# Optimization experiments

Measured on AMD Instinct MI355X. Metric: run time of the kernel, lower is better.

The kernel has to match this reference:

```python
import jax, jax.numpy as jnp
import numpy as np

START_IDX = 1  # PAD_IDX = 0, END_IDX = 2 (unused in teacher-forcing path)
B, N, F = 16, 49, 1024
H, E, V = 1024, 1024, 15000
S, W = 5, 12


def setup_inputs() -> dict:
    key = jax.random.key(0)
    ks = jax.random.split(key, 16)
    def w(k, shape, s=0.02):
        return jax.random.normal(k, shape, dtype=jnp.float32) * s
    emb = w(ks[0], (V, E)).at[0].set(0.0)  # padding_idx = 0
    return dict(
        features=jax.random.normal(ks[1], (B, N, F), dtype=jnp.float32),
        reports=jax.random.randint(ks[2], (B, S, W), 0, V),
        attn_w1=w(ks[3], (F + H, H)), attn_b1=jnp.zeros((H,), jnp.float32),
        attn_w2=w(ks[4], (H, 1)), attn_b2=jnp.zeros((1,), jnp.float32),
        s_wih=w(ks[5], (4 * H, F)), s_whh=w(ks[6], (4 * H, H)),
        s_bih=jnp.zeros((4 * H,), jnp.float32), s_bhh=jnp.zeros((4 * H,), jnp.float32),
        stop_w=w(ks[7], (H, 1)), stop_b=jnp.zeros((1,), jnp.float32),
        emb=emb,
        w_wih=w(ks[8], (4 * H, E)), w_whh=w(ks[9], (4 * H, H)),
        w_bih=jnp.zeros((4 * H,), jnp.float32), w_bhh=jnp.zeros((4 * H,), jnp.float32),
        fc_w=w(ks[10], (H, V)), fc_b=jnp.zeros((V,), jnp.float32),
    )


def _lstm_cell(x, h, c, wih, whh, bih, bhh):
    # PyTorch LSTMCell: gates ordered i, f, g, o
    gates = x @ wih.T + h @ whh.T + (bih + bhh)
    i, f, g, o = jnp.split(gates, 4, axis=-1)
    c = jax.nn.sigmoid(f) * c + jax.nn.sigmoid(i) * jnp.tanh(g)
    h = jax.nn.sigmoid(o) * jnp.tanh(c)
    return h, c


def _attention(features, h, w1, b1, w2, b2):
    # features [B,N,F], h [B,H] -> additive 2-layer attention over N locations
    b, n, _ = features.shape
    hcat = jnp.broadcast_to(h[:, None, :], (b, n, h.shape[-1]))
    x = jnp.concatenate([features, hcat], axis=-1)           # [B,N,F+H]
    e = (jnp.tanh(x @ w1 + b1) @ w2 + b2)[..., 0]            # [B,N]
    scores = jax.nn.softmax(e, axis=-1)
    att = jnp.einsum('bn,bnf->bf', scores, features)          # [B,F]
    return att, scores


def _forward(features, reports, attn_w1, attn_b1, attn_w2, attn_b2,
             s_wih, s_whh, s_bih, s_bhh, stop_w, stop_b, emb,
             w_wih, w_whh, w_bih, w_bhh, fc_w, fc_b):
    bsz = features.shape[0]
    h0 = jnp.zeros((bsz, s_whh.shape[-1]), features.dtype)
    att0, _ = _attention(features, h0, attn_w1, attn_b1, attn_w2, attn_b2)
    start_emb = jnp.broadcast_to(emb[START_IDX][None, :], (bsz, emb.shape[-1]))

    def sentence_step(carry, reports_i):   # reports_i: [W, B] teacher-forcing tokens
        h, c, att = carry
        h, c = _lstm_cell(att, h, c, s_wih, s_whh, s_bih, s_bhh)
        czero = jnp.zeros_like(h)

        def word_step(wc, idx):
            hw, cw, inp = wc
            hw, cw = _lstm_cell(inp, hw, cw, w_wih, w_whh, w_bih, w_bhh)
            pred = hw @ fc_w + fc_b                           # [B,V]
            return (hw, cw, emb[idx]), pred

        # word LSTM initialized with h=topic, c=0; first input = <start> embedding
        _, preds = jax.lax.scan(word_step, (h, czero, start_emb), reports_i)  # [W,B,V]
        stop = jax.nn.sigmoid(h @ stop_w + stop_b)[:, 0]      # [B]
        att, scores = _attention(features, h, attn_w1, attn_b1, attn_w2, attn_b2)
        return (h, c, att), (preds, stop, scores)

    reports_sw = jnp.transpose(reports, (1, 2, 0))            # [S,W,B]
    _, (seq, stops, scores) = jax.lax.scan(sentence_step, (h0, h0, att0), reports_sw)
    seq_out = jnp.transpose(seq, (2, 0, 1, 3))                # [B,S,W,V]
    stops_out = jnp.transpose(stops, (1, 0))                  # [B,S]
    scores_out = jnp.transpose(scores, (1, 0, 2))             # [B,S,N]
    return seq_out, stops_out, scores_out


def reference(features, reports, attn_w1, attn_b1, attn_w2, attn_b2,
              s_wih, s_whh, s_bih, s_bhh, stop_w, stop_b, emb,
              w_wih, w_whh, w_bih, w_bhh, fc_w, fc_b):
    return _forward(features, reports, attn_w1, attn_b1, attn_w2, attn_b2,
                    s_wih, s_whh, s_bih, s_bhh, stop_w, stop_b, emb,
                    w_wih, w_whh, w_bih, w_bhh, fc_w, fc_b)
```

## Files before the change

kernel.cpp:

```cpp
#include <hip/hip_runtime.h>
#include <hip/hip_bf16.h>

#define B_  16
#define S_  5
#define W_  12
#define NL_ 49
#define H_  1024
#define V_  15000
#define SEQ_N   14400000
#define STOP_N  80
#define OUT_STOP (SEQ_N)
#define OUT_SCORE (SEQ_N + STOP_N)

typedef __attribute__((ext_vector_type(8))) short     short8;
typedef __attribute__((ext_vector_type(4))) float     f32x4;
typedef __attribute__((ext_vector_type(4))) unsigned int u32x4;
typedef __attribute__((ext_vector_type(4))) unsigned short us4;

#define OFF_FCWT   0ull
#define OFF_WWHHP  30720000ull
#define OFF_WWIHP  39108608ull
#define OFF_WSCATP 47497216ull
#define OFF_W1AT   64274432ull
#define OFF_W1BT   66371584ull
#define OFF_FBF    68468736ull
#define OFF_XIN    70074368ull
#define OFF_PF     72040448ull
#define OFF_XW     75251712ull
#define OFF_HBALL  90980352ull
#define OFF_HWBF0  92946432ull
#define OFF_HWBF1  93110272ull
#define OFF_ACAT1  93274112ull
#define OFF_H      93339648ull
#define OFF_EVAL   93405184ull
#define OFF_ACAT0  93408384ull
#define OFF_C      93473920ull
#define OFF_CW     93539456ull
#define OFF_HPROJ  93867136ull
#define WS_TOTAL   93932672ull
#define ZERO_BASE  OFF_ACAT0
#define ZERO_BYTES (524288ull)

__device__ __forceinline__ unsigned short f2bf(float x){
  unsigned u = __float_as_uint(x);
  u += 0x7fffu + ((u >> 16) & 1u);
  return (unsigned short)(u >> 16);
}
__device__ __forceinline__ float sigm(float x){ return 1.f/(1.f+expf(-x)); }

typedef __attribute__((address_space(3))) unsigned int  as3_u32;
typedef __attribute__((address_space(1))) const unsigned int as1_u32;

__device__ __forceinline__ void gl16(const void* g, void* l){
  __builtin_amdgcn_global_load_lds((as1_u32*)g, (as3_u32*)l, 16, 0, 0);
}

template<int ROWS,int CH,int NW>
__device__ __forceinline__ void stage_swz(const unsigned short* __restrict__ gbase, int grs,
                                          unsigned short* lds, int wid, int lane,
                                          int r0, int rmax){
  constexpr int RPI = 64/CH;
  constexpr int NISS = ROWS/RPI;
  const int r_in = lane / CH;
  const int cbp  = lane % CH;
  #pragma unroll
  for (int it = wid; it < NISS; it += NW){
    int rl = it*RPI + r_in;
    int gr = r0 + rl; gr = gr < rmax ? gr : rmax-1;
    int cb = cbp ^ (rl & 7);
    gl16(gbase + (size_t)gr*grs + cb*8, lds + it*RPI*CH*8);
  }
}

__global__ void k_cvt(const float* __restrict__ src, unsigned short* __restrict__ dst, int n){
  int idx = (blockIdx.x*256 + threadIdx.x)*4;
  if (idx >= n) return;
  f32x4 v = *(const f32x4*)(src + idx);
  us4 o; o[0]=f2bf(v[0]); o[1]=f2bf(v[1]); o[2]=f2bf(v[2]); o[3]=f2bf(v[3]);
  *(us4*)(dst + idx) = o;
}

__global__ void k_cvt_gate(const float* __restrict__ src, unsigned short* __restrict__ dst,
                           int dld, int doff){
  int idx = (blockIdx.x*256 + threadIdx.x)*4;
  int n = idx >> 10, cc = idx & 1023;
  int gate = (n >> 4) & 3, j = ((n >> 6) << 4) | (n & 15);
  f32x4 v = *(const f32x4*)(src + ((size_t)(gate*1024 + j) << 10) + cc);
  us4 o; o[0]=f2bf(v[0]); o[1]=f2bf(v[1]); o[2]=f2bf(v[2]); o[3]=f2bf(v[3]);
  *(us4*)(dst + (size_t)n*dld + doff + cc) = o;
}

__global__ void k_transp(const float* __restrict__ src, int sld, int r0, int R, int Cc,
                         unsigned short* __restrict__ dst, int dld){
  __shared__ float t[32][33];
  int rb = blockIdx.x*32, cb = blockIdx.y*32;
  int tx = threadIdx.x & 31, ty = threadIdx.x >> 5;
  for (int i = ty; i < 32; i += 8){
    int r = rb + i, c = cb + tx;
    t[i][tx] = (r < R && c < Cc) ? src[(size_t)(r0 + r)*sld + c] : 0.f;
  }
  __syncthreads();
  for (int i = ty; i < 32; i += 8){
    int c = cb + i, r = rb + tx;
    if (c < Cc && r < R) dst[(size_t)c*dld + r] = f2bf(t[tx][i]);
  }
}

__global__ void k_gather(const float* __restrict__ emb, const int* __restrict__ reports,
                         unsigned short* __restrict__ Xin){
  int m = blockIdx.x;
  int w = m / 80, r = m % 80, s = r >> 4, b = r & 15;
  int tok = (w == 0) ? 1 : reports[b*60 + s*12 + (w-1)];
  const float* src = emb + ((size_t)tok << 10);
  int k = threadIdx.x * 4;
  f32x4 v = *(const f32x4*)(src + k);
  us4 o; o[0]=f2bf(v[0]); o[1]=f2bf(v[1]); o[2]=f2bf(v[2]); o[3]=f2bf(v[3]);
  *(us4*)(Xin + (size_t)m*1024 + k) = o;
}

template<int BM,int BN,int BK,int WM,int WN,int EPI>
__global__ void k_gemm(const unsigned short* __restrict__ A, int lda,
                       const unsigned short* __restrict__ Bt, int ldb,
                       float* __restrict__ C, int ldc,
                       const float* __restrict__ bias,
                       int M, int N, int K)
{
  constexpr int NWV = WM*WN;
  constexpr int CH = BK/8;
  __shared__ __align__(16) unsigned short As[BM*BK];
  __shared__ __align__(16) unsigned short Bs[BN*BK];
  const int n0 = blockIdx.x * BN, m0 = blockIdx.y * BM;
  if (n0 >= N) return;
  const int tid  = threadIdx.x;
  const int lane = tid & 63;
  const int wave = tid >> 6;
  constexpr int WROWS = BM/WM, WCOLS = BN/WN;
  constexpr int FM = WROWS/16, FN = WCOLS/16;
  const int wm = wave / WN, wn = wave % WN;
  const int g = lane >> 4, fr = lane & 15;
  const int sx = fr & 7;

  f32x4 acc[FM][FN];
  #pragma unroll
  for (int a=0;a<FM;a++)
    #pragma unroll
    for (int b=0;b<FN;b++) acc[a][b] = (f32x4){0.f,0.f,0.f,0.f};

  for (int k0 = 0; k0 < K; k0 += BK) {
    if (k0) __syncthreads();
    stage_swz<BM,CH,NWV>(A + k0, lda, As, wave, lane, m0, M);
    stage_swz<BN,CH,NWV>(Bt + k0, ldb, Bs, wave, lane, n0, N);
    __syncthreads();
    #pragma unroll
    for (int kk = 0; kk < BK; kk += 32) {
      const int so = ((kk/8 + g) ^ sx) * 8;
      short8 af[FM], bt[FN];
      #pragma unroll
      for (int fm=0; fm<FM; fm++)
        af[fm] = *(const short8*)(As + (wm*WROWS + fm*16 + fr)*BK + so);
      #pragma unroll
      for (int fn=0; fn<FN; fn++)
        bt[fn] = *(const short8*)(Bs + (wn*WCOLS + fn*16 + fr)*BK + so);
      #pragma unroll
      for (int fm=0; fm<FM; fm++)
        #pragma unroll
        for (int fn=0; fn<FN; fn++)
          acc[fm][fn] = __builtin_amdgcn_mfma_f32_16x16x32_bf16(af[fm], bt[fn], acc[fm][fn], 0, 0, 0);
    }
  }

  #pragma unroll
  for (int fm=0; fm<FM; fm++)
    #pragma unroll
    for (int fn=0; fn<FN; fn++)
      #pragma unroll
      for (int j=0; j<4; j++){
        int m = m0 + wm*WROWS + fm*16 + g*4 + j;
        int n = n0 + wn*WCOLS + fn*16 + fr;
        if (m < M && n < N) {
          float v = acc[fm][fn][j];
          if (EPI == 1 || EPI == 2) v += bias[n];
          if (EPI == 2) {
            int b = m & 15, s = (m >> 4) % 5, w = m / 80;
            __builtin_nontemporal_store(v, &C[(size_t)((b*5 + s)*12 + w)*V_ + n]);
          } else if (EPI == 3) {
            __builtin_nontemporal_store(v, &C[(size_t)m*ldc + n]);
          } else {
            C[(size_t)m*ldc + n] = v;
          }
        }
      }
}

template<int BM,int BN,int BK,int WN,int SENT>
__global__ void k_gemm_cell(const unsigned short* __restrict__ A, int lda,
                            const unsigned short* __restrict__ Bt, int ldb,
                            const float* __restrict__ Xg, int ldx,
                            const float* __restrict__ bih, const float* __restrict__ bhh,
                            float* __restrict__ cst,
                            unsigned short* __restrict__ h1, int ldh1,
                            unsigned short* __restrict__ h2,
                            float* __restrict__ hf,
                            int M, int K)
{
  constexpr int CH = BK/8;
  __shared__ __align__(16) unsigned short As[BM*BK];
  __shared__ __align__(16) unsigned short Bs[BN*BK];
  const int tid  = threadIdx.x;
  const int lane = tid & 63;
  const int wn   = tid >> 6;
  const int n0 = blockIdx.x * BN, m0 = blockIdx.y * BM;
  const int g = lane >> 4, fr = lane & 15;
  const int sx = fr & 7;

  f32x4 acc[4];
  #pragma unroll
  for (int b=0;b<4;b++) acc[b] = (f32x4){0.f,0.f,0.f,0.f};

  for (int k0 = 0; k0 < K; k0 += BK) {
    if (k0) __syncthreads();
    stage_swz<BM,CH,WN>(A + k0, lda, As, wn, lane, m0, M);
    stage_swz<BN,CH,WN>(Bt + k0, ldb, Bs, wn, lane, n0, 4096);
    __syncthreads();
    #pragma unroll
    for (int kk = 0; kk < BK; kk += 32) {
      const int so = ((kk/8 + g) ^ sx) * 8;
      short8 af = *(const short8*)(As + fr*BK + so);
      #pragma unroll
      for (int fn=0; fn<4; fn++){
        short8 bt = *(const short8*)(Bs + (wn*64 + fn*16 + fr)*BK + so);
        acc[fn] = __builtin_amdgcn_mfma_f32_16x16x32_bf16(af, bt, acc[fn], 0, 0, 0);
      }
    }
  }

  const int nb = n0 + wn*64 + fr;
  const int j  = ((n0 + wn*64) >> 2) + fr;
  const float b0 = bih[j]        + bhh[j];
  const float b1 = bih[1024 + j] + bhh[1024 + j];
  const float b2 = bih[2048 + j] + bhh[2048 + j];
  const float b3 = bih[3072 + j] + bhh[3072 + j];
  #pragma unroll
  for (int jj=0; jj<4; jj++){
    int m = m0 + g*4 + jj;
    if (m < M){
      float gi = acc[0][jj] + b0;
      float gf = acc[1][jj] + b1;
      float gg = acc[2][jj] + b2;
      float go = acc[3][jj] + b3;
      if (!SENT){
        const float* xg = Xg + (size_t)m*ldx + nb;
        gi += xg[0]; gf += xg[16]; gg += xg[32]; go += xg[48];
      }
      float cn = sigm(gf)*cst[m*1024 + j] + sigm(gi)*tanhf(gg);
      float hn = sigm(go)*tanhf(cn);
      cst[m*1024 + j] = cn;
      unsigned short hb = f2bf(hn);
      h1[(size_t)m*ldh1 + j] = hb;
      h2[(size_t)m*1024 + j] = hb;
      if (SENT) hf[m*1024 + j] = hn;
    }
  }
}

__global__ void k_attn_e(const float* __restrict__ PF, const float* __restrict__ hproj,
                         const float* __restrict__ w2, float* __restrict__ evals)
{
  const int bn = blockIdx.x;
  const int b  = bn / NL_;
  const int tid = threadIdx.x;
  __shared__ float red[4];
  const float* pf = PF + ((size_t)bn << 10);
  const float* hp = hproj + (b << 10);
  int k = tid * 4;
  f32x4 a = *(const f32x4*)(pf + k);
  f32x4 hh = *(const f32x4*)(hp + k);
  f32x4 w = *(const f32x4*)(w2 + k);
  float p = tanhf(a[0]+hh[0])*w[0] + tanhf(a[1]+hh[1])*w[1]
          + tanhf(a[2]+hh[2])*w[2] + tanhf(a[3]+hh[3])*w[3];
  #pragma unroll
  for (int o = 32; o; o >>= 1) p += __shfl_down(p, o, 64);
  if ((tid & 63) == 0) red[tid >> 6] = p;
  __syncthreads();
  if (tid == 0) evals[bn] = red[0] + red[1] + red[2] + red[3];
}

template<int INIT>
__global__ void k_attn_fin(const float* __restrict__ evals, const float* __restrict__ features,
                           const float* __restrict__ h, const float* __restrict__ stop_w,
                           const float* __restrict__ stop_b,
                           unsigned short* __restrict__ Acat, float* __restrict__ outp, int s)
{
  const int b = blockIdx.x, tid = threadIdx.x;
  __shared__ float scs[64];
  __shared__ float red[4];
  if (tid < 64){
    float e = (tid < NL_) ? evals[b*NL_ + tid] : -1e30f;
    float mx = e;
    #pragma unroll
    for (int o = 32; o; o >>= 1) mx = fmaxf(mx, __shfl_xor(mx, o, 64));
    float ex = (tid < NL_) ? expf(e - mx) : 0.f;
    float dn = ex;
    #pragma unroll
    for (int o = 32; o; o >>= 1) dn += __shfl_xor(dn, o, 64);
    float sc = ex / dn;
    if (tid < NL_){
      scs[tid] = sc;
      if (!INIT) outp[OUT_SCORE + (b*5 + s)*NL_ + tid] = sc;
    }
  }
  __syncthreads();
  {
    int f0 = tid * 4;
    f32x4 a = (f32x4){0.f,0.f,0.f,0.f};
    const float* fb = features + (((size_t)b*NL_) << 10) + f0;
    #pragma unroll 7
    for (int n = 0; n < NL_; n++){
      f32x4 v = *(const f32x4*)(fb + ((size_t)n << 10));
      float sc = scs[n];
      a[0] += sc*v[0]; a[1] += sc*v[1]; a[2] += sc*v[2]; a[3] += sc*v[3];
    }
    us4 o4; o4[0]=f2bf(a[0]); o4[1]=f2bf(a[1]); o4[2]=f2bf(a[2]); o4[3]=f2bf(a[3]);
    *(us4*)(Acat + b*2048 + f0) = o4;
  }
  if (!INIT){
    int k = tid * 4;
    f32x4 hv = *(const f32x4*)(h + (b << 10) + k);
    f32x4 sw = *(const f32x4*)(stop_w + k);
    float p = hv[0]*sw[0] + hv[1]*sw[1] + hv[2]*sw[2] + hv[3]*sw[3];
    #pragma unroll
    for (int o = 32; o; o >>= 1) p += __shfl_down(p, o, 64);
    if ((tid & 63) == 0) red[tid >> 6] = p;
    __syncthreads();
    if (tid == 0) outp[OUT_STOP + b*5 + s] = sigm(red[0]+red[1]+red[2]+red[3] + stop_b[0]);
  }
}

extern "C" void kernel_launch(void* const* d_in, const int* in_sizes, int n_in,
                              void* d_out, int out_size, void* d_ws, size_t ws_size,
                              hipStream_t stream)
{
  const float* features = (const float*)d_in[0];
  const int*   reports  = (const int*)d_in[1];
  const float* attn_w1  = (const float*)d_in[2];
  const float* attn_b1  = (const float*)d_in[3];
  const float* attn_w2  = (const float*)d_in[4];
  const float* s_wih    = (const float*)d_in[6];
  const float* s_whh    = (const float*)d_in[7];
  const float* s_bih    = (const float*)d_in[8];
  const float* s_bhh    = (const float*)d_in[9];
  const float* stop_w   = (const float*)d_in[10];
  const float* stop_b   = (const float*)d_in[11];
  const float* emb      = (const float*)d_in[12];
  const float* w_wih    = (const float*)d_in[13];
  const float* w_whh    = (const float*)d_in[14];
  const float* w_bih    = (const float*)d_in[15];
  const float* w_bhh    = (const float*)d_in[16];
  const float* fc_w     = (const float*)d_in[17];
  const float* fc_b     = (const float*)d_in[18];
  float* out = (float*)d_out;
  char*  ws  = (char*)d_ws;
  if (ws_size < WS_TOTAL) return;

  unsigned short* FCWT   = (unsigned short*)(ws + OFF_FCWT);
  unsigned short* WWHHP  = (unsigned short*)(ws + OFF_WWHHP);
  unsigned short* WWIHP  = (unsigned short*)(ws + OFF_WWIHP);
  unsigned short* WSCATP = (unsigned short*)(ws + OFF_WSCATP);
  unsigned short* W1AT   = (unsigned short*)(ws + OFF_W1AT);
  unsigned short* W1BT   = (unsigned short*)(ws + OFF_W1BT);
  unsigned short* FBF    = (unsigned short*)(ws + OFF_FBF);
  unsigned short* XIN    = (unsigned short*)(ws + OFF_XIN);
  float*          PF     = (float*)(ws + OFF_PF);
  float*          XW     = (float*)(ws + OFF_XW);
  unsigned short* HBALL  = (unsigned short*)(ws + OFF_HBALL);
  unsigned short* HW0    = (unsigned short*)(ws + OFF_HWBF0);
  unsigned short* HW1    = (unsigned short*)(ws + OFF_HWBF1);
  unsigned short* ACAT0  = (unsigned short*)(ws + OFF_ACAT0);
  unsigned short* ACAT1  = (unsigned short*)(ws + OFF_ACAT1);
  float*          Hst    = (float*)(ws + OFF_H);
  float*          Cst    = (float*)(ws + OFF_C);
  float*          CW     = (float*)(ws + OFF_CW);
  float*          HPROJ  = (float*)(ws + OFF_HPROJ);
  float*          EVAL   = (float*)(ws + OFF_EVAL);

  hipMemsetAsync(ws + ZERO_BASE, 0, ZERO_BYTES, stream);

  k_cvt<<<784, 256, 0, stream>>>(features, FBF, 802816);
  k_cvt_gate<<<4096, 256, 0, stream>>>(w_whh, WWHHP, 1024, 0);
  k_cvt_gate<<<4096, 256, 0, stream>>>(w_wih, WWIHP, 1024, 0);
  k_cvt_gate<<<4096, 256, 0, stream>>>(s_wih, WSCATP, 2048, 0);
  k_cvt_gate<<<4096, 256, 0, stream>>>(s_whh, WSCATP, 2048, 1024);
  k_transp<<<dim3(32,32),  256, 0, stream>>>(attn_w1, 1024, 0,    1024, 1024,  W1AT, 1024);
  k_transp<<<dim3(32,32),  256, 0, stream>>>(attn_w1, 1024, 1024, 1024, 1024,  W1BT, 1024);
  k_transp<<<dim3(32,469), 256, 0, stream>>>(fc_w,   15000, 0,    1024, 15000, FCWT, 1024);
  k_gather<<<960, 256, 0, stream>>>(emb, reports, XIN);

  k_gemm<64,64,128,2,2,1><<<dim3(16,13), 256, 0, stream>>>(FBF,1024, W1AT,1024, PF,1024, attn_b1, 784,1024,1024);
  k_gemm<64,128,128,2,2,3><<<dim3(32,15), 256, 0, stream>>>(XIN,1024, WWIHP,1024, XW,4096, nullptr, 960,4096,1024);

  k_attn_e<<<784, 256, 0, stream>>>(PF, HPROJ, attn_w2, EVAL);
  k_attn_fin<1><<<16, 256, 0, stream>>>(EVAL, features, Hst, stop_w, stop_b, ACAT0, out, 0);

  unsigned short* ACS[2] = {ACAT0, ACAT1};
  for (int s = 0; s < S_; s++){
    unsigned short* cur = ACS[s & 1];
    unsigned short* nxt = ACS[(s + 1) & 1];
    k_gemm_cell<16,128,128,2,1><<<dim3(32,1), 128, 0, stream>>>(
        cur, 2048, WSCATP, 2048, nullptr, 0, s_bih, s_bhh, Cst,
        nxt + 1024, 2048, HW0 + s*16*1024, Hst, 16, 2048);
    k_gemm<16,64,256,1,4,0><<<dim3(16,1), 256, 0, stream>>>(
        nxt + 1024, 2048, W1BT, 1024, HPROJ, 1024, nullptr, 16, 1024, 1024);
    k_attn_e<<<784, 256, 0, stream>>>(PF, HPROJ, attn_w2, EVAL);
    k_attn_fin<0><<<16, 256, 0, stream>>>(EVAL, features, Hst, stop_w, stop_b, nxt, out, s);
  }

  unsigned short* HW[2] = {HW0, HW1};
  for (int w = 0; w < W_; w++){
    k_gemm_cell<16,128,128,2,0><<<dim3(32,5), 128, 0, stream>>>(
        HW[w & 1], 1024, WWHHP, 1024, XW + (size_t)w*80*4096, 4096, w_bih, w_bhh, CW,
        HW[(w + 1) & 1], 1024, HBALL + (size_t)w*80*1024, nullptr, 80, 1024);
  }

  k_gemm<128,128,64,2,2,2><<<dim3(120,8), 256, 0, stream>>>(HBALL,1024, FCWT,1024, out,V_, fc_b, 960,15000,1024);
}
```

Measured before the change: 559.1 us.

## Fuse prep kernels and run word LSTM as persistent kernel with grid barrier

Merges the feature, gate-weight and embedding conversion kernels into one launch and the two attn_w1 transposes into one. Replaces the 12 per-step word LSTM launches with one persistent kernel of 160 blocks that syncs through a global atomic barrier, whose counters are zeroed by the existing memset. Also changes the final FC GEMM tile shape and grid, and removes the n0 >= N early exit from k_gemm. The barrier assumes all 160 blocks are resident at once and adds spin-wait cost in exchange for removing launch gaps.

Measured after the change: 658.9 us. 17.9% more time.

```diff
diff --git a/kernel.cpp b/kernel.cpp
--- a/kernel.cpp
+++ b/kernel.cpp
@@ -37,9 +37,10 @@
 #define OFF_C      93473920ull
 #define OFF_CW     93539456ull
 #define OFF_HPROJ  93867136ull
-#define WS_TOTAL   93932672ull
+#define OFF_BAR    93932672ull
+#define WS_TOTAL   93932928ull
 #define ZERO_BASE  OFF_ACAT0
-#define ZERO_BYTES (524288ull)
+#define ZERO_BYTES (524544ull)
 
 __device__ __forceinline__ unsigned short f2bf(float x){
   unsigned u = __float_as_uint(x);
@@ -72,22 +73,74 @@
   }
 }
 
-__global__ void k_cvt(const float* __restrict__ src, unsigned short* __restrict__ dst, int n){
-  int idx = (blockIdx.x*256 + threadIdx.x)*4;
-  if (idx >= n) return;
-  f32x4 v = *(const f32x4*)(src + idx);
-  us4 o; o[0]=f2bf(v[0]); o[1]=f2bf(v[1]); o[2]=f2bf(v[2]); o[3]=f2bf(v[3]);
-  *(us4*)(dst + idx) = o;
-}
-
-__global__ void k_cvt_gate(const float* __restrict__ src, unsigned short* __restrict__ dst,
-                           int dld, int doff){
-  int idx = (blockIdx.x*256 + threadIdx.x)*4;
+__device__ __forceinline__ void gbar(unsigned* c, unsigned tgt){
+  __syncthreads();
+  if (threadIdx.x == 0){
+    __threadfence();
+    atomicAdd(c, 1u);
+    while (atomicAdd(c, 0u) < tgt) __builtin_amdgcn_s_sleep(8);
+    __threadfence();
+  }
+  __syncthreads();
+}
+
+__device__ __forceinline__ void cvt_gate_blk(const float* __restrict__ src,
+                                             unsigned short* __restrict__ dst,
+                                             int blk, int dld, int doff){
+  int idx = (blk*256 + threadIdx.x)*4;
   int n = idx >> 10, cc = idx & 1023;
   int gate = (n >> 4) & 3, j = ((n >> 6) << 4) | (n & 15);
   f32x4 v = *(const f32x4*)(src + ((size_t)(gate*1024 + j) << 10) + cc);
   us4 o; o[0]=f2bf(v[0]); o[1]=f2bf(v[1]); o[2]=f2bf(v[2]); o[3]=f2bf(v[3]);
   *(us4*)(dst + (size_t)n*dld + doff + cc) = o;
+}
+
+__global__ void k_prep(const float* __restrict__ features,
+                       const float* __restrict__ w_whh, const float* __restrict__ w_wih,
+                       const float* __restrict__ s_wih, const float* __restrict__ s_whh,
+                       const float* __restrict__ emb, const int* __restrict__ reports,
+                       unsigned short* __restrict__ FBF, unsigned short* __restrict__ WWHHP,
+                       unsigned short* __restrict__ WWIHP, unsigned short* __restrict__ WSCATP,
+                       unsigned short* __restrict__ XIN)
+{
+  int bx = blockIdx.x;
+  if (bx < 784){
+    int idx = (bx*256 + threadIdx.x)*4;
+    f32x4 v = *(const f32x4*)(features + idx);
+    us4 o; o[0]=f2bf(v[0]); o[1]=f2bf(v[1]); o[2]=f2bf(v[2]); o[3]=f2bf(v[3]);
+    *(us4*)(FBF + idx) = o;
+  } else if (bx < 784 + 4096){
+    cvt_gate_blk(w_whh, WWHHP, bx - 784, 1024, 0);
+  } else if (bx < 784 + 8192){
+    cvt_gate_blk(w_wih, WWIHP, bx - (784 + 4096), 1024, 0);
+  } else if (bx < 784 + 12288){
+    cvt_gate_blk(s_wih, WSCATP, bx - (784 + 8192), 2048, 0);
+  } else if (bx < 784 + 16384){
+    cvt_gate_blk(s_whh, WSCATP, bx - (784 + 12288), 2048, 1024);
+  } else {
+    int m = bx - (784 + 16384);
+    int w = m / 80, r = m % 80, s = r >> 4, b = r & 15;
+    int tok = (w == 0) ? 1 : reports[b*60 + s*12 + (w-1)];
+    const float* src = emb + ((size_t)tok << 10);
+    int k = threadIdx.x * 4;
+    f32x4 v = *(const f32x4*)(src + k);
+    us4 o; o[0]=f2bf(v[0]); o[1]=f2bf(v[1]); o[2]=f2bf(v[2]); o[3]=f2bf(v[3]);
+    *(us4*)(XIN + (size_t)m*1024 + k) = o;
+  }
+}
+
+__global__ void k_transp_w1(const float* __restrict__ src,
+                            unsigned short* __restrict__ W1AT, unsigned short* __restrict__ W1BT){
+  __shared__ float t[32][33];
+  unsigned short* dst = blockIdx.z ? W1BT : W1AT;
+  int r0 = blockIdx.z * 1024;
+  int rb = blockIdx.x*32, cb = blockIdx.y*32;
+  int tx = threadIdx.x & 31, ty = threadIdx.x >> 5;
+  for (int i = ty; i < 32; i += 8)
+    t[i][tx] = src[(size_t)(r0 + rb + i)*1024 + cb + tx];
+  __syncthreads();
+  for (int i = ty; i < 32; i += 8)
+    dst[(size_t)(cb + i)*1024 + rb + tx] = f2bf(t[tx][i]);
 }
 
 __global__ void k_transp(const float* __restrict__ src, int sld, int r0, int R, int Cc,
@@ -106,18 +159,6 @@
   }
 }
 
-__global__ void k_gather(const float* __restrict__ emb, const int* __restrict__ reports,
-                         unsigned short* __restrict__ Xin){
-  int m = blockIdx.x;
-  int w = m / 80, r = m % 80, s = r >> 4, b = r & 15;
-  int tok = (w == 0) ? 1 : reports[b*60 + s*12 + (w-1)];
-  const float* src = emb + ((size_t)tok << 10);
-  int k = threadIdx.x * 4;
-  f32x4 v = *(const f32x4*)(src + k);
-  us4 o; o[0]=f2bf(v[0]); o[1]=f2bf(v[1]); o[2]=f2bf(v[2]); o[3]=f2bf(v[3]);
-  *(us4*)(Xin + (size_t)m*1024 + k) = o;
-}
-
 template<int BM,int BN,int BK,int WM,int WN,int EPI>
 __global__ void k_gemm(const unsigned short* __restrict__ A, int lda,
                        const unsigned short* __restrict__ Bt, int ldb,
@@ -130,7 +171,6 @@
   __shared__ __align__(16) unsigned short As[BM*BK];
   __shared__ __align__(16) unsigned short Bs[BN*BK];
   const int n0 = blockIdx.x * BN, m0 = blockIdx.y * BM;
-  if (n0 >= N) return;
   const int tid  = threadIdx.x;
   const int lane = tid & 63;
   const int wave = tid >> 6;
@@ -192,16 +232,15 @@
       }
 }
 
-template<int BM,int BN,int BK,int WN,int SENT>
-__global__ void k_gemm_cell(const unsigned short* __restrict__ A, int lda,
-                            const unsigned short* __restrict__ Bt, int ldb,
-                            const float* __restrict__ Xg, int ldx,
-                            const float* __restrict__ bih, const float* __restrict__ bhh,
-                            float* __restrict__ cst,
-                            unsigned short* __restrict__ h1, int ldh1,
-                            unsigned short* __restrict__ h2,
-                            float* __restrict__ hf,
-                            int M, int K)
+template<int BM,int BN,int BK,int WN>
+__global__ void k_gemm_cell_s(const unsigned short* __restrict__ A, int lda,
+                              const unsigned short* __restrict__ Bt, int ldb,
+                              const float* __restrict__ bih, const float* __restrict__ bhh,
+                              float* __restrict__ cst,
+                              unsigned short* __restrict__ h1, int ldh1,
+                              unsigned short* __restrict__ h2,
+                              float* __restrict__ hf,
+                              int M, int K)
 {
   constexpr int CH = BK/8;
   __shared__ __align__(16) unsigned short As[BM*BK];
@@ -234,7 +273,6 @@
     }
   }
 
-  const int nb = n0 + wn*64 + fr;
   const int j  = ((n0 + wn*64) >> 2) + fr;
   const float b0 = bih[j]        + bhh[j];
   const float b1 = bih[1024 + j] + bhh[1024 + j];
@@ -248,18 +286,85 @@
       float gf = acc[1][jj] + b1;
       float gg = acc[2][jj] + b2;
       float go = acc[3][jj] + b3;
-      if (!SENT){
-        const float* xg = Xg + (size_t)m*ldx + nb;
-        gi += xg[0]; gf += xg[16]; gg += xg[32]; go += xg[48];
-      }
       float cn = sigm(gf)*cst[m*1024 + j] + sigm(gi)*tanhf(gg);
       float hn = sigm(go)*tanhf(cn);
       cst[m*1024 + j] = cn;
       unsigned short hb = f2bf(hn);
       h1[(size_t)m*ldh1 + j] = hb;
       h2[(size_t)m*1024 + j] = hb;
-      if (SENT) hf[m*1024 + j] = hn;
-    }
+      hf[m*1024 + j] = hn;
+    }
+  }
+}
+
+__global__ void __launch_bounds__(128) k_word_chain(
+    const unsigned short* __restrict__ Bt,
+    const float* __restrict__ XW,
+    const float* __restrict__ bih, const float* __restrict__ bhh,
+    float* __restrict__ cw,
+    unsigned short* __restrict__ HW0,
+    unsigned short* __restrict__ HW1,
+    unsigned short* __restrict__ Hball,
+    unsigned* __restrict__ bar)
+{
+  constexpr int BK = 128, CH = BK/8;
+  __shared__ __align__(16) unsigned short As[16*BK];
+  __shared__ __align__(16) unsigned short Bs[128*BK];
+  const int tid = threadIdx.x, lane = tid & 63, wn = tid >> 6;
+  const int n0 = blockIdx.x * 128, m0 = blockIdx.y * 16;
+  const int g = lane >> 4, fr = lane & 15, sx = fr & 7;
+  const unsigned tgt = 160;
+
+  const int nb = n0 + wn*64 + fr;
+  const int j  = ((n0 + wn*64) >> 2) + fr;
+  const float b0 = bih[j]        + bhh[j];
+  const float b1 = bih[1024 + j] + bhh[1024 + j];
+  const float b2 = bih[2048 + j] + bhh[2048 + j];
+  const float b3 = bih[3072 + j] + bhh[3072 + j];
+
+  unsigned short* HW[2] = {HW0, HW1};
+
+  for (int w = 0; w < W_; w++){
+    const unsigned short* A = HW[w & 1];
+    f32x4 acc[4];
+    #pragma unroll
+    for (int b=0;b<4;b++) acc[b] = (f32x4){0.f,0.f,0.f,0.f};
+
+    for (int k0 = 0; k0 < 1024; k0 += BK) {
+      if (k0) __syncthreads();
+      stage_swz<16,CH,2>(A + k0, 1024, As, wn, lane, m0, 80);
+      stage_swz<128,CH,2>(Bt + k0, 1024, Bs, wn, lane, n0, 4096);
+      __syncthreads();
+      #pragma unroll
+      for (int kk = 0; kk < BK; kk += 32) {
+        const int so = ((kk/8 + g) ^ sx) * 8;
+        short8 af = *(const short8*)(As + fr*BK + so);
+        #pragma unroll
+        for (int fn=0; fn<4; fn++){
+          short8 bt = *(const short8*)(Bs + (wn*64 + fn*16 + fr)*BK + so);
+          acc[fn] = __builtin_amdgcn_mfma_f32_16x16x32_bf16(af, bt, acc[fn], 0, 0, 0);
+        }
+      }
+    }
+
+    unsigned short* hnext = HW[(w + 1) & 1];
+    unsigned short* hb_out = Hball + (size_t)w*80*1024;
+    #pragma unroll
+    for (int jj=0; jj<4; jj++){
+      int m = m0 + g*4 + jj;
+      const float* xg = XW + (size_t)(w*80 + m)*4096 + nb;
+      float gi = acc[0][jj] + b0 + xg[0];
+      float gf = acc[1][jj] + b1 + xg[16];
+      float gg = acc[2][jj] + b2 + xg[32];
+      float go = acc[3][jj] + b3 + xg[48];
+      float cn = sigm(gf)*cw[m*1024 + j] + sigm(gi)*tanhf(gg);
+      float hn = sigm(go)*tanhf(cn);
+      cw[m*1024 + j] = cn;
+      unsigned short hb = f2bf(hn);
+      hnext[(size_t)m*1024 + j] = hb;
+      hb_out[(size_t)m*1024 + j] = hb;
+    }
+    if (w < W_ - 1) gbar(bar + w, tgt);
   }
 }
 
@@ -382,18 +487,14 @@
   float*          CW     = (float*)(ws + OFF_CW);
   float*          HPROJ  = (float*)(ws + OFF_HPROJ);
   float*          EVAL   = (float*)(ws + OFF_EVAL);
+  unsigned*       BAR    = (unsigned*)(ws + OFF_BAR);
 
   hipMemsetAsync(ws + ZERO_BASE, 0, ZERO_BYTES, stream);
 
-  k_cvt<<<784, 256, 0, stream>>>(features, FBF, 802816);
-  k_cvt_gate<<<4096, 256, 0, stream>>>(w_whh, WWHHP, 1024, 0);
-  k_cvt_gate<<<4096, 256, 0, stream>>>(w_wih, WWIHP, 1024, 0);
-  k_cvt_gate<<<4096, 256, 0, stream>>>(s_wih, WSCATP, 2048, 0);
-  k_cvt_gate<<<4096, 256, 0, stream>>>(s_whh, WSCATP, 2048, 1024);
-  k_transp<<<dim3(32,32),  256, 0, stream>>>(attn_w1, 1024, 0,    1024, 1024,  W1AT, 1024);
-  k_transp<<<dim3(32,32),  256, 0, stream>>>(attn_w1, 1024, 1024, 1024, 1024,  W1BT, 1024);
-  k_transp<<<dim3(32,469), 256, 0, stream>>>(fc_w,   15000, 0,    1024, 15000, FCWT, 1024);
-  k_gather<<<960, 256, 0, stream>>>(emb, reports, XIN);
+  k_prep<<<784 + 16384 + 960, 256, 0, stream>>>(features, w_whh, w_wih, s_wih, s_whh,
+                                                emb, reports, FBF, WWHHP, WWIHP, WSCATP, XIN);
+  k_transp_w1<<<dim3(32,32,2), 256, 0, stream>>>(attn_w1, W1AT, W1BT);
+  k_transp<<<dim3(32,469), 256, 0, stream>>>(fc_w, 15000, 0, 1024, 15000, FCWT, 1024);
 
   k_gemm<64,64,128,2,2,1><<<dim3(16,13), 256, 0, stream>>>(FBF,1024, W1AT,1024, PF,1024, attn_b1, 784,1024,1024);
   k_gemm<64,128,128,2,2,3><<<dim3(32,15), 256, 0, stream>>>(XIN,1024, WWIHP,1024, XW,4096, nullptr, 960,4096,1024);
@@ -405,8 +506,8 @@
   for (int s = 0; s < S_; s++){
     unsigned short* cur = ACS[s & 1];
     unsigned short* nxt = ACS[(s + 1) & 1];
-    k_gemm_cell<16,128,128,2,1><<<dim3(32,1), 128, 0, stream>>>(
-        cur, 2048, WSCATP, 2048, nullptr, 0, s_bih, s_bhh, Cst,
+    k_gemm_cell_s<16,128,128,2><<<dim3(32,1), 128, 0, stream>>>(
+        cur, 2048, WSCATP, 2048, s_bih, s_bhh, Cst,
         nxt + 1024, 2048, HW0 + s*16*1024, Hst, 16, 2048);
     k_gemm<16,64,256,1,4,0><<<dim3(16,1), 256, 0, stream>>>(
         nxt + 1024, 2048, W1BT, 1024, HPROJ, 1024, nullptr, 16, 1024, 1024);
@@ -414,12 +515,7 @@
     k_attn_fin<0><<<16, 256, 0, stream>>>(EVAL, features, Hst, stop_w, stop_b, nxt, out, s);
   }
 
-  unsigned short* HW[2] = {HW0, HW1};
-  for (int w = 0; w < W_; w++){
-    k_gemm_cell<16,128,128,2,0><<<dim3(32,5), 128, 0, stream>>>(
-        HW[w & 1], 1024, WWHHP, 1024, XW + (size_t)w*80*4096, 4096, w_bih, w_bhh, CW,
-        HW[(w + 1) & 1], 1024, HBALL + (size_t)w*80*1024, nullptr, 80, 1024);
-  }
-
-  k_gemm<128,128,64,2,2,2><<<dim3(120,8), 256, 0, stream>>>(HBALL,1024, FCWT,1024, out,V_, fc_b, 960,15000,1024);
-}
+  k_word_chain<<<dim3(32,5), 128, 0, stream>>>(WWHHP, XW, w_bih, w_bhh, CW, HW0, HW1, HBALL, BAR);
+
+  k_gemm<64,128,64,2,2,2><<<dim3(118,15), 256, 0, stream>>>(HBALL,1024, FCWT,1024, out,V_, fc_b, 960,15000,1024);
+}
```
